# Kernel optimization log

Measured on AMD Instinct MI355X. Metric: run time of the kernel, lower is better.

The kernel has to match this reference:

```python
import jax, jax.numpy as jnp
import numpy as np

B, S, DIM = 256, 196, 768      # batch, seq_len, embed_dim
POOL, LEN, TOPK = 1024, 8, 8   # pool_size, prompt length, top_k


def _l2_normalize(x, axis):
    square_sum = jnp.sum(x * x, axis=axis, keepdims=True)
    return x * jax.lax.rsqrt(jnp.maximum(square_sum, jnp.asarray(1e-12, x.dtype)))


def setup_inputs() -> dict:
    key = jax.random.key(0)
    k1, k2, k3 = jax.random.split(key, 3)
    x_embed = jax.random.normal(k1, (B, S, DIM), dtype=jnp.float32)
    # prompt_init='uniform' -> uniform(-1, 1)
    prompt = jax.random.uniform(k2, (POOL, LEN, DIM), dtype=jnp.float32, minval=-1.0, maxval=1.0)
    prompt_key = jax.random.uniform(k3, (POOL, DIM), dtype=jnp.float32, minval=-1.0, maxval=1.0)
    return {"x_embed": x_embed, "prompt": prompt, "prompt_key": prompt_key}


def reference(x_embed, prompt, prompt_key):
    bsz = x_embed.shape[0]
    # embedding_key == 'mean'
    x_embed_mean = jnp.mean(x_embed, axis=1)                      # [B, D]
    prompt_norm = _l2_normalize(prompt_key, axis=1)               # [P, D]
    x_embed_norm = _l2_normalize(x_embed_mean, axis=1)            # [B, D]
    similarity = jnp.einsum('bd,pd->bp', x_embed_norm, prompt_norm)  # [B, P]
    _, idx = jax.lax.top_k(similarity, TOPK)                      # [B, K]
    # batchwise_prompt: consensus over the batch (unique+counts == bincount over pool)
    id_counts = jnp.zeros((POOL,), jnp.int32).at[idx.ravel()].add(1)
    _, major_prompt_id = jax.lax.top_k(id_counts, TOPK)           # [K]
    idx = jnp.broadcast_to(major_prompt_id[None, :], (bsz, TOPK)) # [B, K]
    batched_prompt = prompt[idx].reshape(bsz, TOPK * LEN, DIM)    # [B, K*L, D]
    batched_key_norm = prompt_norm[idx]                           # [B, K, D]
    reduce_sim = jnp.sum(batched_key_norm * x_embed_norm[:, None, :]) / bsz
    prompted_embedding = jnp.concatenate([batched_prompt, x_embed], axis=1)  # [B, K*L+S, D]
    return prompted_embedding, reduce_sim, similarity, idx
```

## Files before the change

kernel.cpp:

```cpp
#include <hip/hip_runtime.h>
#include <math.h>

#define B_    256
#define S_    196
#define DIM_  768
#define D4_   192
#define POOL_ 1024
#define LEN_  8
#define TOPK_ 8

#define RS_OFF     51118080L
#define SIM_OFF    51118081L
#define IDX_OFF    51380225L

#define WS_XNORM   0L
#define WS_PNORMT  196608L
#define WS_ROWIDS  983040L
#define WS_MAJOR   985088L
#define WS_ROOT    985096L

__global__ void __launch_bounds__(768) prep_kernel(
        const float4* __restrict__ x4,
        const float4* __restrict__ pk4,
        float4* __restrict__ out4,
        float4* __restrict__ xnorm4,
        float* __restrict__ pT,
        int* __restrict__ root) {
    __shared__ float4 part[768];
    __shared__ float  sred[192];
    __shared__ float  sscale;
    __shared__ float  wss[12];
    int t = threadIdx.x;
    if (blockIdx.x == 0 && t == 0) *root = 0;
    if (blockIdx.x < B_) {
        int b = blockIdx.x;
        const float4* xr = x4 + (long)b * (S_ * D4_);
        float4* ow = out4 + ((long)b * 260 + 64) * D4_;
        float4 acc = {0.f, 0.f, 0.f, 0.f};
        #pragma unroll 7
        for (int k = 0; k < 49; ++k) {
            int i = t + k * 768;
            float4 v = xr[i];
            acc.x += v.x; acc.y += v.y; acc.z += v.z; acc.w += v.w;
            ow[i] = v;
        }
        part[t] = acc;
        __syncthreads();
        float4 m = {0.f, 0.f, 0.f, 0.f};
        if (t < 192) {
            float4 a = part[t], b1 = part[t + 192], c1 = part[t + 384], d1 = part[t + 576];
            m.x = (a.x + b1.x + c1.x + d1.x) / 196.f;
            m.y = (a.y + b1.y + c1.y + d1.y) / 196.f;
            m.z = (a.z + b1.z + c1.z + d1.z) / 196.f;
            m.w = (a.w + b1.w + c1.w + d1.w) / 196.f;
            sred[t] = m.x * m.x + m.y * m.y + m.z * m.z + m.w * m.w;
        }
        __syncthreads();
        if (t < 64) {
            float s2 = sred[t] + sred[t + 64] + sred[t + 128];
            #pragma unroll
            for (int off = 32; off > 0; off >>= 1) s2 += __shfl_xor(s2, off);
            if (t == 0) sscale = 1.0f / sqrtf(fmaxf(s2, 1e-12f));
        }
        __syncthreads();
        if (t < 192) {
            float sc = sscale;
            float4 o = {m.x * sc, m.y * sc, m.z * sc, m.w * sc};
            xnorm4[(long)b * D4_ + t] = o;
        }
    } else {
        int r0 = (blockIdx.x - B_) * 4;
        int g = t / 192, i = t % 192;
        int r = r0 + g;
        float4 v = pk4[(long)r * D4_ + i];
        float ss = v.x * v.x + v.y * v.y + v.z * v.z + v.w * v.w;
        #pragma unroll
        for (int off = 32; off > 0; off >>= 1) ss += __shfl_xor(ss, off);
        if ((t & 63) == 0) wss[t >> 6] = ss;
        __syncthreads();
        float tot = wss[3 * g] + wss[3 * g + 1] + wss[3 * g + 2];
        float sc = 1.0f / sqrtf(fmaxf(tot, 1e-12f));
        int d = i * 4;
        pT[(long)d       * POOL_ + r] = v.x * sc;
        pT[(long)(d + 1) * POOL_ + r] = v.y * sc;
        pT[(long)(d + 2) * POOL_ + r] = v.z * sc;
        pT[(long)(d + 3) * POOL_ + r] = v.w * sc;
    }
}

__global__ void __launch_bounds__(512) sim_kernel(
        const float4* __restrict__ xnorm4,
        const float4* __restrict__ pT4,
        float4* __restrict__ sim4) {
    __shared__ float4 xs4[768];
    __shared__ float4 red4[7 * 256];
    int bg = blockIdx.x;
    int pc = blockIdx.y;
    int t  = threadIdx.x;
    int q64 = t & 63;
    int ds  = t >> 6;
    {
        int i = t;
        xs4[i] = xnorm4[(long)(bg * 4 + i / 192) * D4_ + (i % 192)];
        i = t + 512;
        if (i < 768)
            xs4[i] = xnorm4[(long)(bg * 4 + i / 192) * D4_ + (i % 192)];
    }
    __syncthreads();
    float4 a0 = {0,0,0,0}, a1 = {0,0,0,0}, a2 = {0,0,0,0}, a3 = {0,0,0,0};
    const float4* pbase = pT4 + ((long)ds * 96) * 256 + pc * 64 + q64;
    int xq = ds * 24;
    #pragma unroll 3
    for (int q = 0; q < 24; ++q) {
        float4 xa = xs4[xq + q];
        float4 xb = xs4[192 + xq + q];
        float4 xc = xs4[384 + xq + q];
        float4 xd = xs4[576 + xq + q];
        const float* xaf = (const float*)&xa;
        const float* xbf = (const float*)&xb;
        const float* xcf = (const float*)&xc;
        const float* xdf = (const float*)&xd;
        #pragma unroll
        for (int j = 0; j < 4; ++j) {
            float4 w = pbase[(q * 4 + j) * 256];
            a0.x += xaf[j] * w.x; a0.y += xaf[j] * w.y; a0.z += xaf[j] * w.z; a0.w += xaf[j] * w.w;
            a1.x += xbf[j] * w.x; a1.y += xbf[j] * w.y; a1.z += xbf[j] * w.z; a1.w += xbf[j] * w.w;
            a2.x += xcf[j] * w.x; a2.y += xcf[j] * w.y; a2.z += xcf[j] * w.z; a2.w += xcf[j] * w.w;
            a3.x += xdf[j] * w.x; a3.y += xdf[j] * w.y; a3.z += xdf[j] * w.z; a3.w += xdf[j] * w.w;
        }
    }
    if (ds > 0) {
        int s = ds - 1;
        red4[s * 256 +        q64] = a0;
        red4[s * 256 +  64  + q64] = a1;
        red4[s * 256 + 128  + q64] = a2;
        red4[s * 256 + 192  + q64] = a3;
    }
    __syncthreads();
    if (ds == 0) {
        #pragma unroll
        for (int s = 0; s < 7; ++s) {
            float4 b0 = red4[s * 256 +       q64];
            float4 b1 = red4[s * 256 +  64 + q64];
            float4 b2 = red4[s * 256 + 128 + q64];
            float4 b3 = red4[s * 256 + 192 + q64];
            a0.x += b0.x; a0.y += b0.y; a0.z += b0.z; a0.w += b0.w;
            a1.x += b1.x; a1.y += b1.y; a1.z += b1.z; a1.w += b1.w;
            a2.x += b2.x; a2.y += b2.y; a2.z += b2.z; a2.w += b2.w;
            a3.x += b3.x; a3.y += b3.y; a3.z += b3.z; a3.w += b3.w;
        }
        long base = ((long)(bg * 4)) * 256 + pc * 64 + q64;
        sim4[base]           = a0;
        sim4[base + 256]     = a1;
        sim4[base + 512]     = a2;
        sim4[base + 768]     = a3;
    }
}

__global__ void __launch_bounds__(64) topk_consensus_kernel(
        const float* __restrict__ sim,
        int*   __restrict__ row_ids,
        int*   __restrict__ major,
        float* __restrict__ idx_out,
        float* __restrict__ rs_out,
        int*   __restrict__ root) {
    __shared__ int hist[POOL_];
    __shared__ int majs[TOPK_];
    __shared__ int lastFlag;
    int row  = blockIdx.x;
    int lane = threadIdx.x;
    {
        float v[16];
        const float* r = sim + (long)row * POOL_;
        #pragma unroll
        for (int j = 0; j < 16; ++j) v[j] = r[lane + j * 64];
        for (int it = 0; it < TOPK_; ++it) {
            float bv = v[0];
            int   bi = lane;
            #pragma unroll
            for (int j = 1; j < 16; ++j) {
                if (v[j] > bv) { bv = v[j]; bi = lane + j * 64; }
            }
            #pragma unroll
            for (int off = 32; off > 0; off >>= 1) {
                float ov = __shfl_xor(bv, off);
                int   oi = __shfl_xor(bi, off);
                if (ov > bv || (ov == bv && oi < bi)) { bv = ov; bi = oi; }
            }
            if ((bi & 63) == lane) v[bi >> 6] = -INFINITY;
            if (lane == 0) row_ids[row * TOPK_ + it] = bi;
        }
    }
    if (lane == 0) {
        int prev = __hip_atomic_fetch_add(root, 1, __ATOMIC_ACQ_REL,
                                          __HIP_MEMORY_SCOPE_SYSTEM);
        lastFlag = (prev == B_ - 1);
    }
    __syncthreads();
    if (!lastFlag) return;

    #pragma unroll
    for (int j = 0; j < 16; ++j) hist[lane + j * 64] = 0;
    __syncthreads();
    #pragma unroll
    for (int rr = 0; rr < 4; ++rr) {
        int r = lane + rr * 64;
        #pragma unroll
        for (int j = 0; j < TOPK_; ++j) atomicAdd(&hist[row_ids[r * TOPK_ + j]], 1);
    }
    __syncthreads();
    {
        int v[16];
        #pragma unroll
        for (int j = 0; j < 16; ++j) v[j] = hist[lane + j * 64];
        for (int it = 0; it < TOPK_; ++it) {
            int bv = v[0];
            int bi = lane;
            #pragma unroll
            for (int j = 1; j < 16; ++j) {
                if (v[j] > bv) { bv = v[j]; bi = lane + j * 64; }
            }
            #pragma unroll
            for (int off = 32; off > 0; off >>= 1) {
                int ov = __shfl_xor(bv, off);
                int oi = __shfl_xor(bi, off);
                if (ov > bv || (ov == bv && oi < bi)) { bv = ov; bi = oi; }
            }
            if (lane == 0) { majs[it] = bi; major[it] = bi; }
            if ((bi & 63) == lane) v[bi >> 6] = -1;
        }
    }
    __syncthreads();
    #pragma unroll
    for (int k = 0; k < 32; ++k) {
        int i = lane + k * 64;
        idx_out[i] = (float)majs[i & 7];
    }
    float s = 0.f;
    #pragma unroll
    for (int rr = 0; rr < 4; ++rr) {
        const float* r = sim + (long)(lane + rr * 64) * POOL_;
        #pragma unroll
        for (int k = 0; k < TOPK_; ++k) s += r[majs[k]];
    }
    #pragma unroll
    for (int off = 32; off > 0; off >>= 1) s += __shfl_xor(s, off);
    if (lane == 0) *rs_out = s / (float)B_;
}

__global__ void gather_kernel(const float4* __restrict__ prompt4,
                              const int* __restrict__ major,
                              float4* __restrict__ out4) {
    __shared__ int maj[TOPK_];
    if (threadIdx.x < TOPK_) maj[threadIdx.x] = major[threadIdx.x];
    __syncthreads();
    const long total = (long)B_ * 64 * D4_;
    for (long g = (long)blockIdx.x * blockDim.x + threadIdx.x; g < total;
         g += (long)gridDim.x * blockDim.x) {
        int  d4 = (int)(g % D4_);
        long q  = g / D4_;
        int  kl = (int)(q & 63);
        int  b  = (int)(q >> 6);
        int  pid = maj[kl >> 3];
        int  l   = kl & 7;
        out4[((long)b * 260 + kl) * D4_ + d4] = prompt4[((long)pid * LEN_ + l) * D4_ + d4];
    }
}

extern "C" void kernel_launch(void* const* d_in, const int* in_sizes, int n_in,
                              void* d_out, int out_size, void* d_ws, size_t ws_size,
                              hipStream_t stream) {
    const float4* x4      = (const float4*)d_in[0];
    const float4* prompt4 = (const float4*)d_in[1];
    const float4* pk4     = (const float4*)d_in[2];
    float* out = (float*)d_out;
    float* ws  = (float*)d_ws;

    float4* out4    = (float4*)out;
    float4* xnorm4  = (float4*)(ws + WS_XNORM);
    float*  pT      = ws + WS_PNORMT;
    int*    row_ids = (int*)(ws + WS_ROWIDS);
    int*    major   = (int*)(ws + WS_MAJOR);
    int*    root    = (int*)(ws + WS_ROOT);
    float*  out_rs  = out + RS_OFF;
    float*  out_sim = out + SIM_OFF;
    float*  out_idx = out + IDX_OFF;

    prep_kernel<<<512, 768, 0, stream>>>(x4, pk4, out4, xnorm4, pT, root);
    dim3 sg(64, 4);
    sim_kernel<<<sg, 512, 0, stream>>>(xnorm4, (const float4*)pT, (float4*)out_sim);
    topk_consensus_kernel<<<B_, 64, 0, stream>>>(out_sim, row_ids, major,
                                                 out_idx, out_rs, root);
    gather_kernel<<<2048, 256, 0, stream>>>(prompt4, major, out4);
}
```

Measured before the change: 129.2 us.

## Fuse per-chunk top-k into sim kernel and merge consensus with gather

The similarity kernel now also computes a per-row top-8 over each 256-wide pool chunk and writes 32 candidates per row. A single final kernel merges those candidates, builds the consensus histogram and writes the gathered prompts to the output. Every block of that kernel redundantly recomputes the full consensus (256 rows × 32 candidates) so the atomic last-block counter and one kernel launch can go. In exchange, each of the 256 blocks repeats the top-k merge, and the sim kernel's reduction tail becomes longer.

Result: slower. 215.0 us (+66.4%).

```diff
diff --git a/kernel.cpp b/kernel.cpp
--- a/kernel.cpp
+++ b/kernel.cpp
@@ -15,23 +15,20 @@
 
 #define WS_XNORM   0L
 #define WS_PNORMT  196608L
-#define WS_ROWIDS  983040L
-#define WS_MAJOR   985088L
-#define WS_ROOT    985096L
+#define WS_CANDV   983040L
+#define WS_CANDI   991232L
 
 __global__ void __launch_bounds__(768) prep_kernel(
         const float4* __restrict__ x4,
         const float4* __restrict__ pk4,
         float4* __restrict__ out4,
         float4* __restrict__ xnorm4,
-        float* __restrict__ pT,
-        int* __restrict__ root) {
+        float* __restrict__ pT) {
     __shared__ float4 part[768];
     __shared__ float  sred[192];
     __shared__ float  sscale;
     __shared__ float  wss[12];
     int t = threadIdx.x;
-    if (blockIdx.x == 0 && t == 0) *root = 0;
     if (blockIdx.x < B_) {
         int b = blockIdx.x;
         const float4* xr = x4 + (long)b * (S_ * D4_);
@@ -88,10 +85,12 @@
     }
 }
 
-__global__ void __launch_bounds__(512) sim_kernel(
+__global__ void __launch_bounds__(512) sim_cand_kernel(
         const float4* __restrict__ xnorm4,
         const float4* __restrict__ pT4,
-        float4* __restrict__ sim4) {
+        float4* __restrict__ sim4,
+        float* __restrict__ cand_val,
+        int*   __restrict__ cand_idx) {
     __shared__ float4 xs4[768];
     __shared__ float4 red4[7 * 256];
     int bg = blockIdx.x;
@@ -150,66 +149,90 @@
             a3.x += b3.x; a3.y += b3.y; a3.z += b3.z; a3.w += b3.w;
         }
         long base = ((long)(bg * 4)) * 256 + pc * 64 + q64;
-        sim4[base]           = a0;
-        sim4[base + 256]     = a1;
-        sim4[base + 512]     = a2;
-        sim4[base + 768]     = a3;
+        sim4[base]       = a0;
+        sim4[base + 256] = a1;
+        sim4[base + 512] = a2;
+        sim4[base + 768] = a3;
+
+        int lane = q64;
+        int base_idx = pc * 256 + lane * 4;
+        #pragma unroll
+        for (int r = 0; r < 4; ++r) {
+            float4 av = (r == 0) ? a0 : (r == 1) ? a1 : (r == 2) ? a2 : a3;
+            float v0 = av.x, v1 = av.y, v2 = av.z, v3 = av.w;
+            int row = bg * 4 + r;
+            for (int it = 0; it < TOPK_; ++it) {
+                float bv = v0; int bj = 0;
+                if (v1 > bv) { bv = v1; bj = 1; }
+                if (v2 > bv) { bv = v2; bj = 2; }
+                if (v3 > bv) { bv = v3; bj = 3; }
+                int bi = base_idx + bj;
+                #pragma unroll
+                for (int off = 32; off > 0; off >>= 1) {
+                    float ov = __shfl_xor(bv, off);
+                    int   oi = __shfl_xor(bi, off);
+                    if (ov > bv || (ov == bv && oi < bi)) { bv = ov; bi = oi; }
+                }
+                if (lane == 0) {
+                    cand_val[row * 32 + pc * 8 + it] = bv;
+                    cand_idx[row * 32 + pc * 8 + it] = bi;
+                }
+                bool mine = (((bi >> 2) & 63) == lane);
+                int  mj   = bi & 3;
+                v0 = (mine && mj == 0) ? -INFINITY : v0;
+                v1 = (mine && mj == 1) ? -INFINITY : v1;
+                v2 = (mine && mj == 2) ? -INFINITY : v2;
+                v3 = (mine && mj == 3) ? -INFINITY : v3;
+            }
+        }
     }
 }
 
-__global__ void __launch_bounds__(64) topk_consensus_kernel(
+__global__ void __launch_bounds__(1024) final_kernel(
+        const float* __restrict__ cand_val,
+        const int*   __restrict__ cand_idx,
         const float* __restrict__ sim,
-        int*   __restrict__ row_ids,
-        int*   __restrict__ major,
-        float* __restrict__ idx_out,
-        float* __restrict__ rs_out,
-        int*   __restrict__ root) {
-    __shared__ int hist[POOL_];
-    __shared__ int majs[TOPK_];
-    __shared__ int lastFlag;
-    int row  = blockIdx.x;
-    int lane = threadIdx.x;
-    {
-        float v[16];
-        const float* r = sim + (long)row * POOL_;
-        #pragma unroll
-        for (int j = 0; j < 16; ++j) v[j] = r[lane + j * 64];
+        const float4* __restrict__ prompt4,
+        float4* __restrict__ out4,
+        float*  __restrict__ idx_out,
+        float*  __restrict__ rs_out) {
+    __shared__ int   winners[B_ * TOPK_];
+    __shared__ int   hist[POOL_];
+    __shared__ int   majs[TOPK_];
+    __shared__ float redc[256];
+    const int b = blockIdx.x;
+    const int t = threadIdx.x;
+    const int wv = t >> 6, lane = t & 63;
+
+    #pragma unroll 2
+    for (int i = 0; i < 16; ++i) {
+        int r = wv * 16 + i;
+        float cv; int ci;
+        if (lane < 32) {
+            cv = cand_val[r * 32 + lane];
+            ci = cand_idx[r * 32 + lane];
+        } else {
+            cv = -INFINITY;
+            ci = 0x7fffffff;
+        }
         for (int it = 0; it < TOPK_; ++it) {
-            float bv = v[0];
-            int   bi = lane;
-            #pragma unroll
-            for (int j = 1; j < 16; ++j) {
-                if (v[j] > bv) { bv = v[j]; bi = lane + j * 64; }
-            }
+            float bv = cv; int bi = ci;
             #pragma unroll
             for (int off = 32; off > 0; off >>= 1) {
                 float ov = __shfl_xor(bv, off);
                 int   oi = __shfl_xor(bi, off);
                 if (ov > bv || (ov == bv && oi < bi)) { bv = ov; bi = oi; }
             }
-            if ((bi & 63) == lane) v[bi >> 6] = -INFINITY;
-            if (lane == 0) row_ids[row * TOPK_ + it] = bi;
-        }
-    }
-    if (lane == 0) {
-        int prev = __hip_atomic_fetch_add(root, 1, __ATOMIC_ACQ_REL,
-                                          __HIP_MEMORY_SCOPE_SYSTEM);
-        lastFlag = (prev == B_ - 1);
-    }
-    __syncthreads();
-    if (!lastFlag) return;
-
-    #pragma unroll
-    for (int j = 0; j < 16; ++j) hist[lane + j * 64] = 0;
-    __syncthreads();
-    #pragma unroll
-    for (int rr = 0; rr < 4; ++rr) {
-        int r = lane + rr * 64;
-        #pragma unroll
-        for (int j = 0; j < TOPK_; ++j) atomicAdd(&hist[row_ids[r * TOPK_ + j]], 1);
-    }
-    __syncthreads();
-    {
+            if (lane == 0) winners[r * TOPK_ + it] = bi;
+            if (ci == bi) cv = -INFINITY;
+        }
+    }
+    hist[t] = 0;
+    __syncthreads();
+    atomicAdd(&hist[winners[t]], 1);
+    atomicAdd(&hist[winners[t + 1024]], 1);
+    __syncthreads();
+    if (t < 64) {
         int v[16];
         #pragma unroll
         for (int j = 0; j < 16; ++j) v[j] = hist[lane + j * 64];
@@ -226,44 +249,37 @@
                 int oi = __shfl_xor(bi, off);
                 if (ov > bv || (ov == bv && oi < bi)) { bv = ov; bi = oi; }
             }
-            if (lane == 0) { majs[it] = bi; major[it] = bi; }
+            if (lane == 0) majs[it] = bi;
             if ((bi & 63) == lane) v[bi >> 6] = -1;
         }
     }
     __syncthreads();
-    #pragma unroll
-    for (int k = 0; k < 32; ++k) {
-        int i = lane + k * 64;
-        idx_out[i] = (float)majs[i & 7];
-    }
-    float s = 0.f;
-    #pragma unroll
-    for (int rr = 0; rr < 4; ++rr) {
-        const float* r = sim + (long)(lane + rr * 64) * POOL_;
-        #pragma unroll
-        for (int k = 0; k < TOPK_; ++k) s += r[majs[k]];
-    }
-    #pragma unroll
-    for (int off = 32; off > 0; off >>= 1) s += __shfl_xor(s, off);
-    if (lane == 0) *rs_out = s / (float)B_;
-}
-
-__global__ void gather_kernel(const float4* __restrict__ prompt4,
-                              const int* __restrict__ major,
-                              float4* __restrict__ out4) {
-    __shared__ int maj[TOPK_];
-    if (threadIdx.x < TOPK_) maj[threadIdx.x] = major[threadIdx.x];
-    __syncthreads();
-    const long total = (long)B_ * 64 * D4_;
-    for (long g = (long)blockIdx.x * blockDim.x + threadIdx.x; g < total;
-         g += (long)gridDim.x * blockDim.x) {
-        int  d4 = (int)(g % D4_);
-        long q  = g / D4_;
-        int  kl = (int)(q & 63);
-        int  b  = (int)(q >> 6);
-        int  pid = maj[kl >> 3];
-        int  l   = kl & 7;
-        out4[((long)b * 260 + kl) * D4_ + d4] = prompt4[((long)pid * LEN_ + l) * D4_ + d4];
+    if (b == 0) {
+        for (int i = t; i < B_ * TOPK_; i += 1024) idx_out[i] = (float)majs[i & 7];
+        if (t < 256) {
+            float s = 0.f;
+            const float* r = sim + (long)t * POOL_;
+            #pragma unroll
+            for (int k = 0; k < TOPK_; ++k) s += r[majs[k]];
+            redc[t] = s;
+        }
+        __syncthreads();
+        for (int off = 128; off > 0; off >>= 1) {
+            if (t < off) redc[t] += redc[t + off];
+            __syncthreads();
+        }
+        if (t == 0) *rs_out = redc[0] / (float)B_;
+    }
+    {
+        float4* dst = out4 + (long)b * 260 * D4_;
+        #pragma unroll 4
+        for (int k = 0; k < 12; ++k) {
+            int i = t + k * 1024;
+            int kl = i / 192;
+            int d4 = i % 192;
+            int pid = majs[kl >> 3];
+            dst[i] = prompt4[((long)pid * LEN_ + (kl & 7)) * D4_ + d4];
+        }
     }
 }
 
@@ -276,20 +292,19 @@
     float* out = (float*)d_out;
     float* ws  = (float*)d_ws;
 
-    float4* out4    = (float4*)out;
-    float4* xnorm4  = (float4*)(ws + WS_XNORM);
-    float*  pT      = ws + WS_PNORMT;
-    int*    row_ids = (int*)(ws + WS_ROWIDS);
-    int*    major   = (int*)(ws + WS_MAJOR);
-    int*    root    = (int*)(ws + WS_ROOT);
-    float*  out_rs  = out + RS_OFF;
-    float*  out_sim = out + SIM_OFF;
-    float*  out_idx = out + IDX_OFF;
-
-    prep_kernel<<<512, 768, 0, stream>>>(x4, pk4, out4, xnorm4, pT, root);
+    float4* out4     = (float4*)out;
+    float4* xnorm4   = (float4*)(ws + WS_XNORM);
+    float*  pT       = ws + WS_PNORMT;
+    float*  cand_val = ws + WS_CANDV;
+    int*    cand_idx = (int*)(ws + WS_CANDI);
+    float*  out_rs   = out + RS_OFF;
+    float*  out_sim  = out + SIM_OFF;
+    float*  out_idx  = out + IDX_OFF;
+
+    prep_kernel<<<512, 768, 0, stream>>>(x4, pk4, out4, xnorm4, pT);
     dim3 sg(64, 4);
-    sim_kernel<<<sg, 512, 0, stream>>>(xnorm4, (const float4*)pT, (float4*)out_sim);
-    topk_consensus_kernel<<<B_, 64, 0, stream>>>(out_sim, row_ids, major,
-                                                 out_idx, out_rs, root);
-    gather_kernel<<<2048, 256, 0, stream>>>(prompt4, major, out4);
+    sim_cand_kernel<<<sg, 512, 0, stream>>>(xnorm4, (const float4*)pT,
+                                            (float4*)out_sim, cand_val, cand_idx);
+    final_kernel<<<B_, 1024, 0, stream>>>(cand_val, cand_idx, out_sim, prompt4,
+                                          out4, out_idx, out_rs);
 }
```
